# Kernel tuning notes

Hardware: AMD Instinct MI355X
Metric: run time of the kernel (lower is better)

The kernel has to match this reference:

```python
import jax, jax.numpy as jnp
import numpy as np

B, NP, FIN = 128, 64, 2048   # graphs, nodes per graph, input feat
H, D = 8, 64                 # GAT heads, per-head dim
HD = H * D                   # 512
HID = 1024                   # Set2Set channels (concat of two 512 convs)
R2 = 16.0                    # radius^2 (r=4)
SLOPE = 0.2                  # GATConv leaky_relu slope
EPS = 0.1                    # BatchNorm eps


def setup_inputs() -> dict:
    key = jax.random.key(0)
    ks = jax.random.split(key, 20)
    s = 0.02
    inp = {}
    inp['x'] = jax.random.normal(ks[0], (B * NP, FIN), jnp.float32)
    inp['pos'] = jax.random.uniform(ks[1], (B * NP, 2), jnp.float32) * 20.0
    inp['batch'] = jnp.repeat(jnp.arange(B, dtype=jnp.int32), NP)
    # lin01: Linear(2048,2048,bias=False) + BN(2048, eps=0.1) (eval mode)
    inp['W0'] = jax.random.normal(ks[2], (FIN, 2048), jnp.float32) * s
    inp['bn0_g'] = jnp.ones((2048,), jnp.float32)
    inp['bn0_b'] = jnp.zeros((2048,), jnp.float32)
    inp['bn0_m'] = jnp.zeros((2048,), jnp.float32)
    inp['bn0_v'] = jnp.ones((2048,), jnp.float32)
    # two GATConv(2048, 64, heads=8)
    inp['Wg1'] = jax.random.normal(ks[3], (2048, HD), jnp.float32) * s
    inp['as1'] = jax.random.normal(ks[4], (H, D), jnp.float32) * s
    inp['ad1'] = jax.random.normal(ks[5], (H, D), jnp.float32) * s
    inp['b1'] = jnp.zeros((HD,), jnp.float32)
    inp['Wg2'] = jax.random.normal(ks[6], (2048, HD), jnp.float32) * s
    inp['as2'] = jax.random.normal(ks[7], (H, D), jnp.float32) * s
    inp['ad2'] = jax.random.normal(ks[8], (H, D), jnp.float32) * s
    inp['b2'] = jnp.zeros((HD,), jnp.float32)
    # Set2Set LSTM: 2 layers, input 2*HID, hidden HID
    inp['Wih0'] = jax.random.normal(ks[9], (4 * HID, 2 * HID), jnp.float32) * s
    inp['Whh0'] = jax.random.normal(ks[10], (4 * HID, HID), jnp.float32) * s
    inp['bih0'] = jnp.zeros((4 * HID,), jnp.float32)
    inp['bhh0'] = jnp.zeros((4 * HID,), jnp.float32)
    inp['Wih1'] = jax.random.normal(ks[11], (4 * HID, HID), jnp.float32) * s
    inp['Whh1'] = jax.random.normal(ks[12], (4 * HID, HID), jnp.float32) * s
    inp['bih1'] = jnp.zeros((4 * HID,), jnp.float32)
    inp['bhh1'] = jnp.zeros((4 * HID,), jnp.float32)
    # lin2: Linear(2048,1024,bias=False) + BN(1024, eps=0.1)
    inp['W2'] = jax.random.normal(ks[13], (2 * HID, HID), jnp.float32) * s
    inp['bn2_g'] = jnp.ones((HID,), jnp.float32)
    inp['bn2_b'] = jnp.zeros((HID,), jnp.float32)
    inp['bn2_m'] = jnp.zeros((HID,), jnp.float32)
    inp['bn2_v'] = jnp.ones((HID,), jnp.float32)
    # lin3: Linear(1024, 10)
    inp['W3'] = jax.random.normal(ks[14], (HID, 10), jnp.float32) * s
    inp['b3'] = jnp.zeros((10,), jnp.float32)
    return inp


def _bn(x, g, b, m, v):
    return (x - m) * jax.lax.rsqrt(v + EPS) * g + b


def _gat(xb, adj, Wg, a_src, a_dst, bias):
    # xb: [B, NP, 2048], adj: [B, NP, NP] bool (diag True = self-loops)
    h = (xb @ Wg).reshape(B, NP, H, D)
    es = jnp.einsum('bnhd,hd->bnh', h, a_src)   # source-node score
    ed = jnp.einsum('bnhd,hd->bnh', h, a_dst)   # target-node score
    # e[b, i, j, h]: edge j -> i
    e = jax.nn.leaky_relu(ed[:, :, None, :] + es[:, None, :, :], SLOPE)
    e = jnp.where(adj[..., None], e, -jnp.inf)
    alpha = jax.nn.softmax(e, axis=2)           # softmax over neighbors j
    out = jnp.einsum('bijh,bjhd->bihd', alpha, h).reshape(B, NP, HD)
    return out + bias


def _cell(inp, h, c, Wih, Whh, bih, bhh):
    z = inp @ Wih.T + h @ Whh.T + bih + bhh
    i, f, g, o = jnp.split(z, 4, axis=-1)
    c = jax.nn.sigmoid(f) * c + jax.nn.sigmoid(i) * jnp.tanh(g)
    return jax.nn.sigmoid(o) * jnp.tanh(c), c


def _forward(x, pos, W0, bn0_g, bn0_b, bn0_m, bn0_v,
             Wg1, as1, ad1, b1, Wg2, as2, ad2, b2,
             Wih0, Whh0, bih0, bhh0, Wih1, Whh1, bih1, bhh1,
             W2, bn2_g, bn2_b, bn2_m, bn2_v, W3, b3):
    # radius_graph(r=4) per graph; GATConv re-adds self-loops -> diag True
    p = pos.reshape(B, NP, 2)
    d2 = jnp.sum((p[:, :, None, :] - p[:, None, :, :]) ** 2, axis=-1)
    adj = d2 <= R2
    x = _bn(jax.nn.relu(x @ W0), bn0_g, bn0_b, bn0_m, bn0_v)  # dropout: eval
    xb = x.reshape(B, NP, 2048)
    g1 = jax.nn.relu(_gat(xb, adj, Wg1, as1, ad1, b1))
    g2 = jax.nn.relu(_gat(xb, adj, Wg2, as2, ad2, b2))
    x2 = jnp.concatenate([g1, g2], axis=-1)                   # [B, NP, 1024]
    # Set2Set: processing_steps=2, 2-layer LSTM
    q_star = jnp.zeros((B, 2 * HID), x2.dtype)
    h0 = c0 = h1 = c1 = jnp.zeros((B, HID), x2.dtype)
    for _ in range(2):
        h0, c0 = _cell(q_star, h0, c0, Wih0, Whh0, bih0, bhh0)
        h1, c1 = _cell(h0, h1, c1, Wih1, Whh1, bih1, bhh1)
        e = jnp.einsum('bnd,bd->bn', x2, h1)
        a = jax.nn.softmax(e, axis=1)                         # per-graph softmax
        r = jnp.einsum('bn,bnd->bd', a, x2)
        q_star = jnp.concatenate([h1, r], axis=-1)            # [B, 2048]
    y = _bn(jax.nn.relu(q_star @ W2), bn2_g, bn2_b, bn2_m, bn2_v)
    return y @ W3 + b3                                        # [B, 10] ('A2')


def reference(x, pos, batch, W0, bn0_g, bn0_b, bn0_m, bn0_v,
              Wg1, as1, ad1, b1, Wg2, as2, ad2, b2,
              Wih0, Whh0, bih0, bhh0, Wih1, Whh1, bih1, bhh1,
              W2, bn2_g, bn2_b, bn2_m, bn2_v, W3, b3):
    # batch ids are implicit in the fixed [B, NP] layout
    return _forward(x, pos, W0, bn0_g, bn0_b, bn0_m, bn0_v,
                    Wg1, as1, ad1, b1, Wg2, as2, ad2, b2,
                    Wih0, Whh0, bih0, bhh0, Wih1, Whh1, bih1, bhh1,
                    W2, bn2_g, bn2_b, bn2_m, bn2_v, W3, b3)
```

## Files before the change

kernel.cpp:

```cpp
#include <hip/hip_runtime.h>
#include <hip/hip_bf16.h>

typedef unsigned short u16;
typedef __attribute__((ext_vector_type(8))) short short8;
typedef __attribute__((ext_vector_type(4))) float f32x4;
typedef unsigned long long u64;

#define DI __device__ __forceinline__

DI u16 f2b(float f){
  unsigned u = __float_as_uint(f);
  unsigned r = 0x7fffu + ((u >> 16) & 1u);
  return (u16)((u + r) >> 16);
}
DI float b2f(u16 u){ return __uint_as_float((unsigned)u << 16); }

DI void gl_lds16(const void* g, void* l){
  __builtin_amdgcn_global_load_lds((const __attribute__((address_space(1))) void*)g,
                                   (__attribute__((address_space(3))) void*)l, 16, 0, 0);
}

constexpr size_t O_XBF = 0;
constexpr size_t O_W0T = O_XBF + 33554432;
constexpr size_t O_WGT = O_W0T + 8388608;
constexpr size_t O_W2T = O_WGT + 4194304;
constexpr size_t O_XB  = O_W2T + 4194304;
constexpr size_t O_H   = O_XB  + 33554432;
constexpr size_t O_ES  = O_H   + 33554432;
constexpr size_t O_ED  = O_ES  + 524288;
constexpr size_t O_ADJ = O_ED  + 524288;
constexpr size_t O_SC0 = O_ADJ + 65536;
constexpr size_t O_SH0 = O_SC0 + 8192;
constexpr size_t O_SC2 = O_SH0 + 8192;
constexpr size_t O_SH2 = O_SC2 + 4096;
constexpr size_t O_LB0 = O_SH2 + 4096;
constexpr size_t O_LB1 = O_LB0 + 16384;
constexpr size_t S_AC0 = 0;
constexpr size_t S_AC1 = S_AC0 + 786432;
constexpr size_t S_C0  = S_AC1 + 524288;
constexpr size_t S_C1  = S_C0  + 524288;
constexpr size_t S_H1F = S_C1  + 524288;
constexpr size_t S_ZP  = S_H1F + 524288;
constexpr size_t S_E   = S_ZP  + 16777216;
constexpr size_t S_Z1U = S_E   + 32768;

__global__ __launch_bounds__(256) void setup_all(
    const float* __restrict__ x,
    const float* __restrict__ W0, const float* __restrict__ Wg1,
    const float* __restrict__ Wg2, const float* __restrict__ W2,
    const float* __restrict__ g0, const float* __restrict__ b0, const float* __restrict__ m0, const float* __restrict__ v0,
    const float* __restrict__ g2, const float* __restrict__ b2, const float* __restrict__ m2, const float* __restrict__ v2,
    const float* __restrict__ bih0, const float* __restrict__ bhh0,
    const float* __restrict__ bih1, const float* __restrict__ bhh1,
    const float* __restrict__ pos,
    u16* __restrict__ xbf, u16* __restrict__ w0t, u16* __restrict__ wgt, u16* __restrict__ w2t,
    float* __restrict__ sc0, float* __restrict__ sh0, float* __restrict__ sc2, float* __restrict__ sh2,
    float* __restrict__ lb0, float* __restrict__ lb1, u64* __restrict__ adjm)
{
  __shared__ float tile[32][33];
  __shared__ float px[4][64], py[4][64];
  int bx = blockIdx.x, t = threadIdx.x;
  if(bx < 8192){
    int idx = bx * 256 + t;
    int r = idx >> 8, c8 = (idx & 255) << 3;
    const float* src = x + (size_t)r * 2048 + c8;
    float4 v0 = *(const float4*)src;
    float4 v1 = *(const float4*)(src + 4);
    short8 ov;
    ov[0] = (short)f2b(v0.x); ov[1] = (short)f2b(v0.y); ov[2] = (short)f2b(v0.z); ov[3] = (short)f2b(v0.w);
    ov[4] = (short)f2b(v1.x); ov[5] = (short)f2b(v1.y); ov[6] = (short)f2b(v1.z); ov[7] = (short)f2b(v1.w);
    *(short8*)(xbf + (size_t)r * 2048 + c8) = ov;
  } else if(bx < 16384){
    int bx2 = bx - 8192;
    int cx = bx2 & 127, by = bx2 >> 7;
    const float* src; u16* dst; int C, droff;
    if(cx < 64){      src = W0;  dst = w0t; C = 2048; droff = 0; }
    else if(cx < 80){ src = Wg1; dst = wgt; C = 512;  droff = 0;   cx -= 64; }
    else if(cx < 96){ src = Wg2; dst = wgt; C = 512;  droff = 512; cx -= 80; }
    else {            src = W2;  dst = w2t; C = 1024; droff = 0;   cx -= 96; }
    int c0 = cx * 32, r0 = by * 32;
    int tx = t & 31, ty = t >> 5;
    for(int i = 0; i < 4; i++)
      tile[ty + 8*i][tx] = src[(size_t)(r0 + ty + 8*i) * C + c0 + tx];
    __syncthreads();
    for(int i = 0; i < 4; i++)
      dst[(size_t)(droff + c0 + ty + 8*i) * 2048 + r0 + tx] = f2b(tile[tx][ty + 8*i]);
  } else if(bx < 16400){
    int tt = (bx - 16384) * 256 + t;
    if(tt < 2048){ float s = g0[tt] * rsqrtf(v0[tt] + 0.1f); sc0[tt] = s; sh0[tt] = b0[tt] - m0[tt] * s; }
    if(tt < 1024){ float s = g2[tt] * rsqrtf(v2[tt] + 0.1f); sc2[tt] = s; sh2[tt] = b2[tt] - m2[tt] * s; }
    lb0[tt] = bih0[tt] + bhh0[tt];
    lb1[tt] = bih1[tt] + bhh1[tt];
  } else {
    int w = t >> 6, l = t & 63;
    int g = (bx - 16400) * 4 + w;
    float2 p = ((const float2*)pos)[g * 64 + l];
    px[w][l] = p.x; py[w][l] = p.y;
    __syncthreads();
    float xi = p.x, yi = p.y;
    u64 m = 0;
    for(int j = 0; j < 64; j++){
      float dx = xi - px[w][j], dy = yi - py[w][j];
      if(dx * dx + dy * dy <= 16.0f) m |= (1ull << j);
    }
    adjm[g * 64 + l] = m;
  }
}

#define STAGE_A(buf, half, kt)                                                        \
  { _Pragma("unroll")                                                                 \
    for(int ld = 0; ld < 2; ld++){                                                    \
      int u = ld * 512 + t;                                                           \
      int r = (u >> 3) + (half) * 128, c = u & 7;                                     \
      gl_lds16(A + (size_t)(m0 + r) * K + (kt) * 64 + ((c ^ (r & 7)) << 3),           \
               LA + (buf) * 16384 + ((half) * 1024 + u) * 8);                         \
    } }
#define STAGE_B(buf, half, kt)                                                        \
  { _Pragma("unroll")                                                                 \
    for(int ld = 0; ld < 2; ld++){                                                    \
      int u = ld * 512 + t;                                                           \
      int r = (u >> 3) + (half) * 128, c = u & 7;                                     \
      gl_lds16(Bt + (size_t)(n0 + r) * K + (kt) * 64 + ((c ^ (r & 7)) << 3),          \
               LB + (buf) * 16384 + ((half) * 1024 + u) * 8);                         \
    } }
#define COMPUTE(buf, q)                                                               \
  { if((q) == 0){                                                                     \
      _Pragma("unroll")                                                               \
      for(int nb = 0; nb < 4; nb++)                                                   \
        _Pragma("unroll")                                                             \
        for(int k2 = 0; k2 < 2; k2++){                                                \
          int col = wn + nb * 16 + (l & 15);                                          \
          int kc = k2 * 4 + (l >> 4);                                                 \
          bfr[nb][k2] = Bp[(buf) * 2048 + col * 8 + (kc ^ (col & 7))];                \
        }                                                                             \
    }                                                                                 \
    short8 af[2][2];                                                                  \
    _Pragma("unroll")                                                                 \
    for(int rb = 0; rb < 2; rb++)                                                     \
      _Pragma("unroll")                                                               \
      for(int k2 = 0; k2 < 2; k2++){                                                  \
        int row = wm + (q) * 32 + rb * 16 + (l & 15);                                 \
        int kc = k2 * 4 + (l >> 4);                                                   \
        af[rb][k2] = Ap[(buf) * 2048 + row * 8 + (kc ^ (row & 7))];                   \
      }                                                                               \
    _Pragma("unroll")                                                                 \
    for(int rb = 0; rb < 2; rb++)                                                     \
      _Pragma("unroll")                                                               \
      for(int nb = 0; nb < 4; nb++)                                                   \
        _Pragma("unroll")                                                             \
        for(int k2 = 0; k2 < 2; k2++)                                                 \
          acc[(q) * 2 + rb][nb] = __builtin_amdgcn_mfma_f32_16x16x32_bf16(            \
              af[rb][k2], bfr[nb][k2], acc[(q) * 2 + rb][nb], 0, 0, 0);               \
  }
#define PHASE_BAR() { __builtin_amdgcn_s_barrier(); __builtin_amdgcn_sched_barrier(0); }
#define VM4() { asm volatile("s_waitcnt vmcnt(4)" ::: "memory"); __builtin_amdgcn_sched_barrier(0); }

__global__ __launch_bounds__(512, 2) void gemm8p(
    const u16* __restrict__ A, const u16* __restrict__ Bt, u16* __restrict__ Cb,
    const float* __restrict__ p1, const float* __restrict__ p2,
    int M, int N, int K)
{
  __shared__ alignas(16) u16 LA[2 * 16384];
  __shared__ alignas(16) u16 LB[2 * 16384];
  int m0 = blockIdx.x * 256, n0 = blockIdx.y * 256;
  int t = threadIdx.x, w = t >> 6, l = t & 63;
  int wm = (w >> 2) * 128, wn = (w & 3) * 64;
  int nt = K >> 6, ni = nt >> 1;
  f32x4 acc[8][4];
  #pragma unroll
  for(int a = 0; a < 8; a++)
    #pragma unroll
    for(int b = 0; b < 4; b++) acc[a][b] = {0.f, 0.f, 0.f, 0.f};
  short8 bfr[4][2];
  const short8* Ap = (const short8*)LA;
  const short8* Bp = (const short8*)LB;

  STAGE_A(0, 0, 0); STAGE_A(0, 1, 0); STAGE_B(0, 0, 0); STAGE_B(0, 1, 0);
  STAGE_B(1, 0, 1); STAGE_B(1, 1, 1);
  VM4();
  PHASE_BAR();

  for(int i = 0; i < ni; i++){
    int t1 = 2 * i + 1;
    int t2 = (2 * i + 2 < nt) ? 2 * i + 2 : nt - 1;
    int t3 = (2 * i + 3 < nt) ? 2 * i + 3 : nt - 1;
    STAGE_A(1, 0, t1); STAGE_A(1, 1, t1);
    COMPUTE(0, 0);
    PHASE_BAR();
    STAGE_B(0, 0, t2);
    COMPUTE(0, 1);
    PHASE_BAR();
    STAGE_B(0, 1, t2);
    COMPUTE(0, 2);
    PHASE_BAR();
    COMPUTE(0, 3);
    VM4();
    PHASE_BAR();
    STAGE_A(0, 0, t2);
    COMPUTE(1, 0);
    PHASE_BAR();
    STAGE_A(0, 1, t2);
    COMPUTE(1, 1);
    PHASE_BAR();
    STAGE_B(1, 0, t3);
    COMPUTE(1, 2);
    PHASE_BAR();
    STAGE_B(1, 1, t3);
    COMPUTE(1, 3);
    VM4();
    PHASE_BAR();
  }
  asm volatile("s_waitcnt vmcnt(0)" ::: "memory");

  int cc = n0 + wn + (l & 15);
  int r4 = (l >> 4) << 2;
  #pragma unroll
  for(int ar = 0; ar < 8; ar++)
    #pragma unroll
    for(int nb = 0; nb < 4; nb++)
      #pragma unroll
      for(int r = 0; r < 4; r++){
        int row = m0 + wm + ar * 16 + r4 + r, col = cc + nb * 16;
        float v = acc[ar][nb][r];
        v = fmaxf(v, 0.f) * p1[col] + p2[col];
        Cb[(size_t)row * N + col] = f2b(v);
      }
}

__global__ __launch_bounds__(256) void gemm_bf16(
    const u16* __restrict__ A, const u16* __restrict__ Bt, u16* __restrict__ Cb,
    int M, int N, int K)
{
  constexpr int BM = 128, BN = 128, BK = 64;
  __shared__ alignas(16) u16 Al[BM * BK];
  __shared__ alignas(16) u16 Bl[BN * BK];
  int m0 = blockIdx.x * BM, n0 = blockIdx.y * BN;
  int t = threadIdx.x, w = t >> 6, l = t & 63;
  int wm = (w >> 1) * 64, wn = (w & 1) * 64;
  f32x4 acc[4][4];
  for(int a = 0; a < 4; a++) for(int b = 0; b < 4; b++) acc[a][b] = {0.f, 0.f, 0.f, 0.f};

  const short8* Ap = (const short8*)Al;
  const short8* Bp = (const short8*)Bl;

  for(int k0 = 0; k0 < K; k0 += BK){
    #pragma unroll
    for(int u = t; u < BM * 8; u += 256){
      int r = u >> 3, c = u & 7;
      gl_lds16(A + (size_t)(m0 + r) * K + k0 + ((c ^ (r & 7)) << 3), Al + u * 8);
    }
    #pragma unroll
    for(int u = t; u < BN * 8; u += 256){
      int r = u >> 3, c = u & 7;
      gl_lds16(Bt + (size_t)(n0 + r) * K + k0 + ((c ^ (r & 7)) << 3), Bl + u * 8);
    }
    __syncthreads();
    #pragma unroll
    for(int ks = 0; ks < 2; ks++){
      int kc = ks * 4 + (l >> 4);
      short8 av[4], bv[4];
      #pragma unroll
      for(int mi = 0; mi < 4; mi++){ int r = wm + mi * 16 + (l & 15); av[mi] = Ap[r * 8 + (kc ^ (r & 7))]; }
      #pragma unroll
      for(int ni = 0; ni < 4; ni++){ int r = wn + ni * 16 + (l & 15); bv[ni] = Bp[r * 8 + (kc ^ (r & 7))]; }
      #pragma unroll
      for(int mi = 0; mi < 4; mi++)
        #pragma unroll
        for(int ni = 0; ni < 4; ni++)
          acc[mi][ni] = __builtin_amdgcn_mfma_f32_16x16x32_bf16(av[mi], bv[ni], acc[mi][ni], 0, 0, 0);
    }
    __syncthreads();
  }

  int cr = m0 + wm + ((l >> 4) << 2);
  int cc = n0 + wn + (l & 15);
  for(int mi = 0; mi < 4; mi++)
    for(int ni = 0; ni < 4; ni++)
      for(int r = 0; r < 4; r++){
        int row = cr + mi * 16 + r, col = cc + ni * 16;
        Cb[(size_t)row * N + col] = f2b(acc[mi][ni][r]);
      }
}

__global__ __launch_bounds__(256) void gemm_sk(
    const u16* __restrict__ A, const u16* __restrict__ Bt, float* __restrict__ Cf,
    int N, int lda, int ldb, int kPer)
{
  constexpr int BM = 128, BN = 64, BK = 64;
  __shared__ alignas(16) u16 Al[BM * BK];
  __shared__ alignas(16) u16 Bl[BN * BK];
  int n0 = blockIdx.x * BN;
  int kb = blockIdx.y * kPer;
  float* C = Cf + (size_t)blockIdx.y * 128 * N;
  int t = threadIdx.x, w = t >> 6, l = t & 63;
  int wm = (w >> 1) * 64, wn = (w & 1) * 32;
  f32x4 acc[4][2];
  for(int a = 0; a < 4; a++) for(int b = 0; b < 2; b++) acc[a][b] = {0.f, 0.f, 0.f, 0.f};

  const short8* Ap = (const short8*)Al;
  const short8* Bp = (const short8*)Bl;

  for(int k0 = kb; k0 < kb + kPer; k0 += BK){
    #pragma unroll
    for(int u = t; u < BM * 8; u += 256){
      int r = u >> 3, c = u & 7;
      gl_lds16(A + (size_t)r * lda + k0 + ((c ^ (r & 7)) << 3), Al + u * 8);
    }
    #pragma unroll
    for(int u = t; u < BN * 8; u += 256){
      int r = u >> 3, c = u & 7;
      gl_lds16(Bt + (size_t)(n0 + r) * ldb + k0 + ((c ^ (r & 7)) << 3), Bl + u * 8);
    }
    __syncthreads();
    #pragma unroll
    for(int ks = 0; ks < 2; ks++){
      int kc = ks * 4 + (l >> 4);
      short8 av[4], bv[2];
      #pragma unroll
      for(int mi = 0; mi < 4; mi++){ int r = wm + mi * 16 + (l & 15); av[mi] = Ap[r * 8 + (kc ^ (r & 7))]; }
      #pragma unroll
      for(int ni = 0; ni < 2; ni++){ int r = wn + ni * 16 + (l & 15); bv[ni] = Bp[r * 8 + (kc ^ (r & 7))]; }
      #pragma unroll
      for(int mi = 0; mi < 4; mi++)
        #pragma unroll
        for(int ni = 0; ni < 2; ni++)
          acc[mi][ni] = __builtin_amdgcn_mfma_f32_16x16x32_bf16(av[mi], bv[ni], acc[mi][ni], 0, 0, 0);
    }
    __syncthreads();
  }

  int cr = wm + ((l >> 4) << 2);
  int cc = n0 + wn + (l & 15);
  for(int mi = 0; mi < 4; mi++)
    for(int ni = 0; ni < 2; ni++)
      for(int r = 0; r < 4; r++)
        C[(size_t)(cr + mi * 16 + r) * N + cc + ni * 16] = acc[mi][ni][r];
}

__global__ __launch_bounds__(256) void gemm_skf(
    const u16* __restrict__ A, const float* __restrict__ Wih, const float* __restrict__ Whh,
    float* __restrict__ Cf, int N, int lda, int Kih, int Khh, int kPer)
{
  constexpr int BM = 128, BN = 64, BK = 64;
  __shared__ alignas(16) u16 Al[BM * BK];
  __shared__ alignas(16) u16 Bl[BN * BK];
  int n0 = blockIdx.x * BN;
  int kb = blockIdx.y * kPer;
  float* C = Cf + (size_t)blockIdx.y * 128 * N;
  int t = threadIdx.x, w = t >> 6, l = t & 63;
  int wm = (w >> 1) * 64, wn = (w & 1) * 32;
  f32x4 acc[4][2];
  for(int a = 0; a < 4; a++) for(int b = 0; b < 2; b++) acc[a][b] = {0.f, 0.f, 0.f, 0.f};

  const short8* Ap = (const short8*)Al;
  const short8* Bp = (const short8*)Bl;

  for(int k0 = kb; k0 < kb + kPer; k0 += BK){
    #pragma unroll
    for(int u = t; u < BM * 8; u += 256){
      int r = u >> 3, c = u & 7;
      gl_lds16(A + (size_t)r * lda + k0 + ((c ^ (r & 7)) << 3), Al + u * 8);
    }
    #pragma unroll
    for(int u = t; u < BN * 8; u += 256){
      int r = u >> 3, c = u & 7;
      int gk = k0 + c * 8;
      const float* src = (gk < Kih) ? (Wih + (size_t)(n0 + r) * Kih + gk)
                                    : (Whh + (size_t)(n0 + r) * Khh + (gk - Kih));
      float4 v0 = *(const float4*)src;
      float4 v1 = *(const float4*)(src + 4);
      short8 ov;
      ov[0] = (short)f2b(v0.x); ov[1] = (short)f2b(v0.y); ov[2] = (short)f2b(v0.z); ov[3] = (short)f2b(v0.w);
      ov[4] = (short)f2b(v1.x); ov[5] = (short)f2b(v1.y); ov[6] = (short)f2b(v1.z); ov[7] = (short)f2b(v1.w);
      ((short8*)Bl)[r * 8 + (c ^ (r & 7))] = ov;
    }
    __syncthreads();
    #pragma unroll
    for(int ks = 0; ks < 2; ks++){
      int kc = ks * 4 + (l >> 4);
      short8 av[4], bv[2];
      #pragma unroll
      for(int mi = 0; mi < 4; mi++){ int r = wm + mi * 16 + (l & 15); av[mi] = Ap[r * 8 + (kc ^ (r & 7))]; }
      #pragma unroll
      for(int ni = 0; ni < 2; ni++){ int r = wn + ni * 16 + (l & 15); bv[ni] = Bp[r * 8 + (kc ^ (r & 7))]; }
      #pragma unroll
      for(int mi = 0; mi < 4; mi++)
        #pragma unroll
        for(int ni = 0; ni < 2; ni++)
          acc[mi][ni] = __builtin_amdgcn_mfma_f32_16x16x32_bf16(av[mi], bv[ni], acc[mi][ni], 0, 0, 0);
    }
    __syncthreads();
  }

  int cr = wm + ((l >> 4) << 2);
  int cc = n0 + wn + (l & 15);
  for(int mi = 0; mi < 4; mi++)
    for(int ni = 0; ni < 2; ni++)
      for(int r = 0; r < 4; r++)
        C[(size_t)(cr + mi * 16 + r) * N + cc + ni * 16] = acc[mi][ni][r];
}

__global__ __launch_bounds__(256) void gat_attn2(const u64* __restrict__ adjm,
    const u16* __restrict__ h,
    const float* __restrict__ as1, const float* __restrict__ ad1,
    const float* __restrict__ as2, const float* __restrict__ ad2,
    const float* __restrict__ b1, const float* __restrict__ b2,
    u16* __restrict__ x2b){
  int b = blockIdx.x;
  int cv = blockIdx.y >> 3, hh = blockIdx.y & 7;
  __shared__ float hst[64][64];
  __shared__ float esl[64], edl[64];
  __shared__ u64 adjs[64];
  int t = threadIdx.x, w = t >> 6, l = t & 63;
  {
    int j = t >> 2, d0 = (t & 3) * 16;
    const u16* hr = h + (size_t)(b * 64 + j) * 1024 + cv * 512 + hh * 64 + d0;
    #pragma unroll
    for(int k = 0; k < 16; k++) hst[j][d0 + k] = b2f(hr[k]);
  }
  if(t < 64) adjs[t] = adjm[b * 64 + t];
  __syncthreads();
  float aSl = ((cv ? as2 : as1) + hh * 64)[l];
  float aDl = ((cv ? ad2 : ad1) + hh * 64)[l];
  for(int it = 0; it < 16; it++){
    int j = it * 4 + w;
    float v = hst[j][l];
    float ps = v * aSl, pd = v * aDl;
    for(int o = 32; o; o >>= 1){ ps += __shfl_xor(ps, o); pd += __shfl_xor(pd, o); }
    if(l == 0){ esl[j] = ps; edl[j] = pd; }
  }
  __syncthreads();
  float alphaR[16];
  #pragma unroll
  for(int it = 0; it < 16; it++){
    int i = it * 4 + w;
    bool on = (adjs[i] >> l) & 1;
    float e = edl[i] + esl[l];
    e = e > 0.f ? e : 0.2f * e;
    float mx = on ? e : -1e30f;
    for(int o = 32; o; o >>= 1) mx = fmaxf(mx, __shfl_xor(mx, o));
    float p = on ? __expf(e - mx) : 0.f;
    float s = p;
    for(int o = 32; o; o >>= 1) s += __shfl_xor(s, o);
    alphaR[it] = p / s;
  }
  float accv[16];
  #pragma unroll
  for(int k = 0; k < 16; k++) accv[k] = 0.f;
  #pragma unroll
  for(int j = 0; j < 64; j++){
    float hv = hst[j][l];
    #pragma unroll
    for(int it = 0; it < 16; it++){
      float av = __uint_as_float(__builtin_amdgcn_readlane(__float_as_uint(alphaR[it]), j));
      accv[it] += av * hv;
    }
  }
  float bl = ((cv ? b2 : b1) + hh * 64)[l];
  #pragma unroll
  for(int it = 0; it < 16; it++){
    int i = it * 4 + w;
    x2b[(size_t)(b * 64 + i) * 1024 + cv * 512 + hh * 64 + l] = f2b(fmaxf(accv[it] + bl, 0.f));
  }
}

__global__ __launch_bounds__(256) void s2s0_gemv(const float* __restrict__ Wih1,
    const float* __restrict__ lb1, const float* __restrict__ lb0, float* __restrict__ z1u){
  __shared__ float hs[1024];
  int t = threadIdx.x;
  for(int i = t; i < 1024; i += 256){
    float zi = lb0[i], zg = lb0[2048 + i], zo = lb0[3072 + i];
    float cn = (1.f / (1.f + __expf(-zi))) * tanhf(zg);
    hs[i] = (1.f / (1.f + __expf(-zo))) * tanhf(cn);
  }
  __syncthreads();
  int w = t >> 6, l = t & 63;
  int r = blockIdx.x * 4 + w;
  const float* wr = Wih1 + (size_t)r * 1024;
  float s = 0.f;
  #pragma unroll
  for(int k = 0; k < 16; k++) s += wr[l + 64 * k] * hs[l + 64 * k];
  for(int o = 32; o; o >>= 1) s += __shfl_xor(s, o);
  if(l == 0) z1u[r] = s + lb1[r];
}

__global__ void lstm_gate0(const float* __restrict__ zp, const float* __restrict__ lb,
                           float* __restrict__ c, u16* __restrict__ ac0, u16* __restrict__ ac1,
                           int ns){
  int t = blockIdx.x * 256 + threadIdx.x;
  int b = t >> 10, j = t & 1023;
  size_t base = (size_t)b * 4096;
  float zi = 0, zf = 0, zg = 0, zo = 0;
  for(int s = 0; s < ns; s++){
    const float* zr = zp + (size_t)s * 524288 + base;
    zi += zr[j]; zf += zr[1024 + j]; zg += zr[2048 + j]; zo += zr[3072 + j];
  }
  zi += lb[j]; zf += lb[1024 + j]; zg += lb[2048 + j]; zo += lb[3072 + j];
  float ci = c[t];
  float si = 1.f / (1.f + __expf(-zi)), sf = 1.f / (1.f + __expf(-zf)), so = 1.f / (1.f + __expf(-zo));
  float cn = sf * ci + si * tanhf(zg);
  c[t] = cn;
  u16 hb = f2b(so * tanhf(cn));
  ac0[(size_t)b * 3072 + 2048 + j] = hb;
  ac1[(size_t)b * 2048 + j] = hb;
}

__global__ void lstm_gate1(const float* __restrict__ zp, const float* __restrict__ lb,
                           float* __restrict__ c, float* __restrict__ h1f,
                           u16* __restrict__ ac1, u16* __restrict__ ac0, int ns){
  int t = blockIdx.x * 256 + threadIdx.x;
  int b = t >> 10, j = t & 1023;
  size_t base = (size_t)b * 4096;
  float zi = 0, zf = 0, zg = 0, zo = 0;
  for(int s = 0; s < ns; s++){
    const float* zr = zp + (size_t)s * 524288 + base;
    zi += zr[j]; zf += zr[1024 + j]; zg += zr[2048 + j]; zo += zr[3072 + j];
  }
  zi += lb[j]; zf += lb[1024 + j]; zg += lb[2048 + j]; zo += lb[3072 + j];
  float ci = c[t];
  float si = 1.f / (1.f + __expf(-zi)), sf = 1.f / (1.f + __expf(-zf)), so = 1.f / (1.f + __expf(-zo));
  float cn = sf * ci + si * tanhf(zg);
  c[t] = cn;
  float hn = so * tanhf(cn);
  h1f[t] = hn;
  u16 hb = f2b(hn);
  ac1[(size_t)b * 2048 + 1024 + j] = hb;
  ac0[(size_t)b * 3072 + j] = hb;
}

template<int STEP>
__global__ __launch_bounds__(256) void s2s_e(const u16* __restrict__ x2b,
    const float* __restrict__ h1, const float* __restrict__ z1u, float* __restrict__ e){
  __shared__ float h1s[1024];
  int t = threadIdx.x, w = t >> 6, l = t & 63;
  int node = blockIdx.x * 4 + w;
  int b = node >> 6;
  for(int i = t; i < 1024; i += 256){
    if(STEP == 0){
      float zi = z1u[i], zg = z1u[2048 + i], zo = z1u[3072 + i];
      float cn = (1.f / (1.f + __expf(-zi))) * tanhf(zg);
      h1s[i] = (1.f / (1.f + __expf(-zo))) * tanhf(cn);
    } else {
      h1s[i] = h1[(size_t)b * 1024 + i];
    }
  }
  __syncthreads();
  const u16* xr = x2b + (size_t)node * 1024;
  float s = 0.f;
  #pragma unroll
  for(int k = 0; k < 16; k++){
    int d = k * 64 + l;
    s += b2f(xr[d]) * h1s[d];
  }
  for(int o = 32; o; o >>= 1) s += __shfl_xor(s, o);
  if(l == 0) e[node] = s;
}

template<int STEP>
__global__ __launch_bounds__(256) void s2s_r(const u16* __restrict__ x2b,
    const float* __restrict__ e, u16* __restrict__ ac0,
    const float* __restrict__ lb0, const float* __restrict__ z1u,
    u16* __restrict__ ac1, float* __restrict__ c0b, float* __restrict__ c1b){
  int b = blockIdx.x, sl = blockIdx.y;
  __shared__ float al[64];
  int t = threadIdx.x;
  if(t < 64){
    float v = e[b * 64 + t];
    float mx = v;
    for(int o = 32; o; o >>= 1) mx = fmaxf(mx, __shfl_xor(mx, o));
    float p = __expf(v - mx);
    float ss = p;
    for(int o = 32; o; o >>= 1) ss += __shfl_xor(ss, o);
    al[t] = p / ss;
  }
  __syncthreads();
  int d = sl * 256 + t;
  const u16* xp = x2b + (size_t)b * 65536 + d;
  float r = 0.f;
  #pragma unroll 8
  for(int j = 0; j < 64; j++) r += al[j] * b2f(xp[j * 1024]);
  ac0[(size_t)b * 3072 + 1024 + d] = f2b(r);
  if(STEP == 0){
    float zi0 = lb0[d], zg0 = lb0[2048 + d], zo0 = lb0[3072 + d];
    float c0 = (1.f / (1.f + __expf(-zi0))) * tanhf(zg0);
    float h0 = (1.f / (1.f + __expf(-zo0))) * tanhf(c0);
    float zi1 = z1u[d], zg1 = z1u[2048 + d], zo1 = z1u[3072 + d];
    float c1 = (1.f / (1.f + __expf(-zi1))) * tanhf(zg1);
    float h1 = (1.f / (1.f + __expf(-zo1))) * tanhf(c1);
    c0b[(size_t)b * 1024 + d] = c0;
    c1b[(size_t)b * 1024 + d] = c1;
    u16 h0b = f2b(h0), h1b = f2b(h1);
    ac0[(size_t)b * 3072 + d] = h1b;
    ac0[(size_t)b * 3072 + 2048 + d] = h0b;
    ac1[(size_t)b * 2048 + d] = h0b;
    ac1[(size_t)b * 2048 + 1024 + d] = h1b;
  }
}

__global__ __launch_bounds__(256) void lin3(const float* __restrict__ zp2,
    const float* __restrict__ sc2, const float* __restrict__ sh2,
    const float* __restrict__ W3, const float* __restrict__ b3, float* __restrict__ out){
  int b = blockIdx.x;
  __shared__ float yl[1024];
  int t = threadIdx.x, w = t >> 6, l = t & 63;
  for(int d = t; d < 1024; d += 256){
    float v = 0.f;
    for(int s = 0; s < 8; s++) v += zp2[(size_t)s * 131072 + b * 1024 + d];
    yl[d] = fmaxf(v, 0.f) * sc2[d] + sh2[d];
  }
  __syncthreads();
  for(int n = w; n < 10; n += 4){
    float s = 0.f;
    for(int d = l; d < 1024; d += 64) s += yl[d] * W3[d * 10 + n];
    for(int o = 32; o; o >>= 1) s += __shfl_xor(s, o);
    if(l == 0) out[b * 10 + n] = s + b3[n];
  }
}

extern "C" void kernel_launch(void* const* d_in, const int* in_sizes, int n_in,
                              void* d_out, int out_size, void* d_ws, size_t ws_size,
                              hipStream_t stream){
  const float* x    = (const float*)d_in[0];
  const float* pos  = (const float*)d_in[1];
  const float* W0   = (const float*)d_in[3];
  const float* bn0g = (const float*)d_in[4];
  const float* bn0b = (const float*)d_in[5];
  const float* bn0m = (const float*)d_in[6];
  const float* bn0v = (const float*)d_in[7];
  const float* Wg1  = (const float*)d_in[8];
  const float* as1  = (const float*)d_in[9];
  const float* ad1  = (const float*)d_in[10];
  const float* b1   = (const float*)d_in[11];
  const float* Wg2  = (const float*)d_in[12];
  const float* as2  = (const float*)d_in[13];
  const float* ad2  = (const float*)d_in[14];
  const float* b2   = (const float*)d_in[15];
  const float* Wih0 = (const float*)d_in[16];
  const float* Whh0 = (const float*)d_in[17];
  const float* bih0 = (const float*)d_in[18];
  const float* bhh0 = (const float*)d_in[19];
  const float* Wih1 = (const float*)d_in[20];
  const float* Whh1 = (const float*)d_in[21];
  const float* bih1 = (const float*)d_in[22];
  const float* bhh1 = (const float*)d_in[23];
  const float* W2   = (const float*)d_in[24];
  const float* bn2g = (const float*)d_in[25];
  const float* bn2b = (const float*)d_in[26];
  const float* bn2m = (const float*)d_in[27];
  const float* bn2v = (const float*)d_in[28];
  const float* W3   = (const float*)d_in[29];
  const float* b3   = (const float*)d_in[30];

  char* ws = (char*)d_ws;
  u16*   xbf  = (u16*)(ws + O_XBF);
  u16*   x2b  = (u16*)(ws + O_XBF);
  u16*   w0t  = (u16*)(ws + O_W0T);
  u16*   wgt  = (u16*)(ws + O_WGT);
  u16*   w2t  = (u16*)(ws + O_W2T);
  u16*   xb   = (u16*)(ws + O_XB);
  u16*   hb   = (u16*)(ws + O_H);
  u64*   adjm = (u64*)(ws + O_ADJ);
  float* sc0  = (float*)(ws + O_SC0);
  float* sh0  = (float*)(ws + O_SH0);
  float* sc2  = (float*)(ws + O_SC2);
  float* sh2  = (float*)(ws + O_SH2);
  float* lb0  = (float*)(ws + O_LB0);
  float* lb1  = (float*)(ws + O_LB1);
  char*  s2sb = ws + O_H;
  u16*   ac0  = (u16*)(s2sb + S_AC0);
  u16*   ac1  = (u16*)(s2sb + S_AC1);
  float* c0b  = (float*)(s2sb + S_C0);
  float* c1b  = (float*)(s2sb + S_C1);
  float* h1f  = (float*)(s2sb + S_H1F);
  float* zp   = (float*)(s2sb + S_ZP);
  float* ebuf = (float*)(s2sb + S_E);
  float* z1u  = (float*)(s2sb + S_Z1U);

  setup_all<<<16432, 256, 0, stream>>>(x, W0, Wg1, Wg2, W2,
                                       bn0g, bn0b, bn0m, bn0v, bn2g, bn2b, bn2m, bn2v,
                                       bih0, bhh0, bih1, bhh1, pos,
                                       xbf, w0t, wgt, w2t, sc0, sh0, sc2, sh2, lb0, lb1, adjm);

  gemm8p<<<dim3(32, 8), 512, 0, stream>>>(xbf, w0t, xb, sc0, sh0, 8192, 2048, 2048);
  gemm_bf16<<<dim3(64, 8), 256, 0, stream>>>(xb, wgt, hb, 8192, 1024, 2048);
  gat_attn2<<<dim3(128, 16), 256, 0, stream>>>(adjm, hb, as1, ad1, as2, ad2, b1, b2, x2b);

  s2s0_gemv<<<1024, 256, 0, stream>>>(Wih1, lb1, lb0, z1u);
  s2s_e<0><<<2048, 256, 0, stream>>>(x2b, nullptr, z1u, ebuf);
  s2s_r<0><<<dim3(128, 4), 256, 0, stream>>>(x2b, ebuf, ac0, lb0, z1u, ac1, c0b, c1b);

  gemm_skf<<<dim3(64, 8), 256, 0, stream>>>(ac0, Wih0, Whh0, zp, 4096, 3072, 2048, 1024, 384);
  lstm_gate0<<<512, 256, 0, stream>>>(zp, lb0, c0b, ac0, ac1, 8);
  gemm_skf<<<dim3(64, 8), 256, 0, stream>>>(ac1, Wih1, Whh1, zp, 4096, 2048, 1024, 1024, 256);
  lstm_gate1<<<512, 256, 0, stream>>>(zp, lb1, c1b, h1f, ac1, ac0, 8);
  s2s_e<1><<<2048, 256, 0, stream>>>(x2b, h1f, nullptr, ebuf);
  s2s_r<1><<<dim3(128, 4), 256, 0, stream>>>(x2b, ebuf, ac0, nullptr, nullptr, nullptr, nullptr, nullptr);

  gemm_sk<<<dim3(16, 8), 256, 0, stream>>>(ac0, w2t, zp, 1024, 3072, 2048, 256);
  lin3<<<128, 256, 0, stream>>>(zp, sc2, sh2, W3, b3, (float*)d_out);
}
```

Before: 277.1 us.

## Use pipelined gemm8p for GAT projection and fold s2s0 gemv into setup

The GAT projection GEMM (8192x1024x2048) now runs on the templated, software-pipelined 256x256-tile gemm8p kernel instead of the simple 128x128 gemm_bf16. Under MODE 3 it skips the relu/BN epilogue. The first-step LSTM gemv that computes z1u is folded into setup_all as extra blocks, which removes one kernel launch. z1u moves to a separate workspace slot so it is not overwritten by the s2s buffers, since setup now writes it before the GEMMs that reuse the O_H region. The larger tile gives only 128 blocks for the second GEMM, so some CUs may sit idle.

```diff
diff --git a/kernel.cpp b/kernel.cpp
--- a/kernel.cpp
+++ b/kernel.cpp
@@ -35,6 +35,7 @@
 constexpr size_t O_SH2 = O_SC2 + 4096;
 constexpr size_t O_LB0 = O_SH2 + 4096;
 constexpr size_t O_LB1 = O_LB0 + 16384;
+constexpr size_t O_Z1U = O_LB1 + 16384;
 constexpr size_t S_AC0 = 0;
 constexpr size_t S_AC1 = S_AC0 + 786432;
 constexpr size_t S_C0  = S_AC1 + 524288;
@@ -42,7 +43,6 @@
 constexpr size_t S_H1F = S_C1  + 524288;
 constexpr size_t S_ZP  = S_H1F + 524288;
 constexpr size_t S_E   = S_ZP  + 16777216;
-constexpr size_t S_Z1U = S_E   + 32768;
 
 __global__ __launch_bounds__(256) void setup_all(
     const float* __restrict__ x,
@@ -52,13 +52,14 @@
     const float* __restrict__ g2, const float* __restrict__ b2, const float* __restrict__ m2, const float* __restrict__ v2,
     const float* __restrict__ bih0, const float* __restrict__ bhh0,
     const float* __restrict__ bih1, const float* __restrict__ bhh1,
-    const float* __restrict__ pos,
+    const float* __restrict__ pos, const float* __restrict__ Wih1,
     u16* __restrict__ xbf, u16* __restrict__ w0t, u16* __restrict__ wgt, u16* __restrict__ w2t,
     float* __restrict__ sc0, float* __restrict__ sh0, float* __restrict__ sc2, float* __restrict__ sh2,
-    float* __restrict__ lb0, float* __restrict__ lb1, u64* __restrict__ adjm)
+    float* __restrict__ lb0, float* __restrict__ lb1, u64* __restrict__ adjm, float* __restrict__ z1u)
 {
   __shared__ float tile[32][33];
   __shared__ float px[4][64], py[4][64];
+  __shared__ float hs[1024];
   int bx = blockIdx.x, t = threadIdx.x;
   if(bx < 8192){
     int idx = bx * 256 + t;
@@ -91,7 +92,7 @@
     if(tt < 1024){ float s = g2[tt] * rsqrtf(v2[tt] + 0.1f); sc2[tt] = s; sh2[tt] = b2[tt] - m2[tt] * s; }
     lb0[tt] = bih0[tt] + bhh0[tt];
     lb1[tt] = bih1[tt] + bhh1[tt];
-  } else {
+  } else if(bx < 16432){
     int w = t >> 6, l = t & 63;
     int g = (bx - 16400) * 4 + w;
     float2 p = ((const float2*)pos)[g * 64 + l];
@@ -104,6 +105,23 @@
       if(dx * dx + dy * dy <= 16.0f) m |= (1ull << j);
     }
     adjm[g * 64 + l] = m;
+  } else {
+    for(int i = t; i < 1024; i += 256){
+      float zi = bih0[i] + bhh0[i];
+      float zg = bih0[2048 + i] + bhh0[2048 + i];
+      float zo = bih0[3072 + i] + bhh0[3072 + i];
+      float cn = (1.f / (1.f + __expf(-zi))) * tanhf(zg);
+      hs[i] = (1.f / (1.f + __expf(-zo))) * tanhf(cn);
+    }
+    __syncthreads();
+    int w = t >> 6, l = t & 63;
+    int r = (bx - 16432) * 4 + w;
+    const float* wr = Wih1 + (size_t)r * 1024;
+    float s = 0.f;
+    #pragma unroll
+    for(int k = 0; k < 16; k++) s += wr[l + 64 * k] * hs[l + 64 * k];
+    for(int o = 32; o; o >>= 1) s += __shfl_xor(s, o);
+    if(l == 0) z1u[r] = s + bih1[r] + bhh1[r];
   }
 }
 
@@ -155,6 +173,7 @@
 #define PHASE_BAR() { __builtin_amdgcn_s_barrier(); __builtin_amdgcn_sched_barrier(0); }
 #define VM4() { asm volatile("s_waitcnt vmcnt(4)" ::: "memory"); __builtin_amdgcn_sched_barrier(0); }
 
+template<int MODE>
 __global__ __launch_bounds__(512, 2) void gemm8p(
     const u16* __restrict__ A, const u16* __restrict__ Bt, u16* __restrict__ Cb,
     const float* __restrict__ p1, const float* __restrict__ p2,
@@ -222,63 +241,8 @@
       for(int r = 0; r < 4; r++){
         int row = m0 + wm + ar * 16 + r4 + r, col = cc + nb * 16;
         float v = acc[ar][nb][r];
-        v = fmaxf(v, 0.f) * p1[col] + p2[col];
+        if(MODE == 1) v = fmaxf(v, 0.f) * p1[col] + p2[col];
         Cb[(size_t)row * N + col] = f2b(v);
-      }
-}
-
-__global__ __launch_bounds__(256) void gemm_bf16(
-    const u16* __restrict__ A, const u16* __restrict__ Bt, u16* __restrict__ Cb,
-    int M, int N, int K)
-{
-  constexpr int BM = 128, BN = 128, BK = 64;
-  __shared__ alignas(16) u16 Al[BM * BK];
-  __shared__ alignas(16) u16 Bl[BN * BK];
-  int m0 = blockIdx.x * BM, n0 = blockIdx.y * BN;
-  int t = threadIdx.x, w = t >> 6, l = t & 63;
-  int wm = (w >> 1) * 64, wn = (w & 1) * 64;
-  f32x4 acc[4][4];
-  for(int a = 0; a < 4; a++) for(int b = 0; b < 4; b++) acc[a][b] = {0.f, 0.f, 0.f, 0.f};
-
-  const short8* Ap = (const short8*)Al;
-  const short8* Bp = (const short8*)Bl;
-
-  for(int k0 = 0; k0 < K; k0 += BK){
-    #pragma unroll
-    for(int u = t; u < BM * 8; u += 256){
-      int r = u >> 3, c = u & 7;
-      gl_lds16(A + (size_t)(m0 + r) * K + k0 + ((c ^ (r & 7)) << 3), Al + u * 8);
-    }
-    #pragma unroll
-    for(int u = t; u < BN * 8; u += 256){
-      int r = u >> 3, c = u & 7;
-      gl_lds16(Bt + (size_t)(n0 + r) * K + k0 + ((c ^ (r & 7)) << 3), Bl + u * 8);
-    }
-    __syncthreads();
-    #pragma unroll
-    for(int ks = 0; ks < 2; ks++){
-      int kc = ks * 4 + (l >> 4);
-      short8 av[4], bv[4];
-      #pragma unroll
-      for(int mi = 0; mi < 4; mi++){ int r = wm + mi * 16 + (l & 15); av[mi] = Ap[r * 8 + (kc ^ (r & 7))]; }
-      #pragma unroll
-      for(int ni = 0; ni < 4; ni++){ int r = wn + ni * 16 + (l & 15); bv[ni] = Bp[r * 8 + (kc ^ (r & 7))]; }
-      #pragma unroll
-      for(int mi = 0; mi < 4; mi++)
-        #pragma unroll
-        for(int ni = 0; ni < 4; ni++)
-          acc[mi][ni] = __builtin_amdgcn_mfma_f32_16x16x32_bf16(av[mi], bv[ni], acc[mi][ni], 0, 0, 0);
-    }
-    __syncthreads();
-  }
-
-  int cr = m0 + wm + ((l >> 4) << 2);
-  int cc = n0 + wn + (l & 15);
-  for(int mi = 0; mi < 4; mi++)
-    for(int ni = 0; ni < 4; ni++)
-      for(int r = 0; r < 4; r++){
-        int row = cr + mi * 16 + r, col = cc + ni * 16;
-        Cb[(size_t)row * N + col] = f2b(acc[mi][ni][r]);
       }
 }
 
@@ -462,26 +426,6 @@
     int i = it * 4 + w;
     x2b[(size_t)(b * 64 + i) * 1024 + cv * 512 + hh * 64 + l] = f2b(fmaxf(accv[it] + bl, 0.f));
   }
-}
-
-__global__ __launch_bounds__(256) void s2s0_gemv(const float* __restrict__ Wih1,
-    const float* __restrict__ lb1, const float* __restrict__ lb0, float* __restrict__ z1u){
-  __shared__ float hs[1024];
-  int t = threadIdx.x;
-  for(int i = t; i < 1024; i += 256){
-    float zi = lb0[i], zg = lb0[2048 + i], zo = lb0[3072 + i];
-    float cn = (1.f / (1.f + __expf(-zi))) * tanhf(zg);
-    hs[i] = (1.f / (1.f + __expf(-zo))) * tanhf(cn);
-  }
-  __syncthreads();
-  int w = t >> 6, l = t & 63;
-  int r = blockIdx.x * 4 + w;
-  const float* wr = Wih1 + (size_t)r * 1024;
-  float s = 0.f;
-  #pragma unroll
-  for(int k = 0; k < 16; k++) s += wr[l + 64 * k] * hs[l + 64 * k];
-  for(int o = 32; o; o >>= 1) s += __shfl_xor(s, o);
-  if(l == 0) z1u[r] = s + lb1[r];
 }
 
 __global__ void lstm_gate0(const float* __restrict__ zp, const float* __restrict__ lb,
@@ -666,6 +610,7 @@
   float* sh2  = (float*)(ws + O_SH2);
   float* lb0  = (float*)(ws + O_LB0);
   float* lb1  = (float*)(ws + O_LB1);
+  float* z1u  = (float*)(ws + O_Z1U);
   char*  s2sb = ws + O_H;
   u16*   ac0  = (u16*)(s2sb + S_AC0);
   u16*   ac1  = (u16*)(s2sb + S_AC1);
@@ -674,18 +619,16 @@
   float* h1f  = (float*)(s2sb + S_H1F);
   float* zp   = (float*)(s2sb + S_ZP);
   float* ebuf = (float*)(s2sb + S_E);
-  float* z1u  = (float*)(s2sb + S_Z1U);
-
-  setup_all<<<16432, 256, 0, stream>>>(x, W0, Wg1, Wg2, W2,
+
+  setup_all<<<16688, 256, 0, stream>>>(x, W0, Wg1, Wg2, W2,
                                        bn0g, bn0b, bn0m, bn0v, bn2g, bn2b, bn2m, bn2v,
-                                       bih0, bhh0, bih1, bhh1, pos,
-                                       xbf, w0t, wgt, w2t, sc0, sh0, sc2, sh2, lb0, lb1, adjm);
-
-  gemm8p<<<dim3(32, 8), 512, 0, stream>>>(xbf, w0t, xb, sc0, sh0, 8192, 2048, 2048);
-  gemm_bf16<<<dim3(64, 8), 256, 0, stream>>>(xb, wgt, hb, 8192, 1024, 2048);
+                                       bih0, bhh0, bih1, bhh1, pos, Wih1,
+                                       xbf, w0t, wgt, w2t, sc0, sh0, sc2, sh2, lb0, lb1, adjm, z1u);
+
+  gemm8p<1><<<dim3(32, 8), 512, 0, stream>>>(xbf, w0t, xb, sc0, sh0, 8192, 2048, 2048);
+  gemm8p<3><<<dim3(32, 4), 512, 0, stream>>>(xb, wgt, hb, nullptr, nullptr, 8192, 1024, 2048);
   gat_attn2<<<dim3(128, 16), 256, 0, stream>>>(adjm, hb, as1, ad1, as2, ad2, b1, b2, x2b);
 
-  s2s0_gemv<<<1024, 256, 0, stream>>>(Wih1, lb1, lb0, z1u);
   s2s_e<0><<<2048, 256, 0, stream>>>(x2b, nullptr, z1u, ebuf);
   s2s_r<0><<<dim3(128, 4), 256, 0, stream>>>(x2b, ebuf, ac0, lb0, z1u, ac1, c0b, c1b);
 
```

Measured after the change: 288.7 us. 4.2% more time.
